# Kernel optimization log

Measured on AMD Instinct MI355X. Metric: run time of the kernel, lower is better.

The kernel has to match this reference:

```python
import jax, jax.numpy as jnp
import numpy as np

NH, NKV, D = 16, 8, 128
HID = 2048
EPS = 1e-6
ROPE_BASE = 10000.0
T = 2048


def setup_inputs() -> dict:
    key = jax.random.key(0)
    k1, k2, k3 = jax.random.split(key, 3)
    return {
        "positions": jnp.arange(T, dtype=jnp.int32),
        "hidden_states": jax.random.normal(k1, (T, HID), dtype=jnp.float32),
        "w_qkv": jax.random.normal(k2, (HID, (NH + 2 * NKV) * D), dtype=jnp.float32) * 0.02,
        "w_o": jax.random.normal(k3, (NH * D, HID), dtype=jnp.float32) * 0.02,
        "q_norm_w": jnp.ones((D,), dtype=jnp.float32),
        "k_norm_w": jnp.ones((D,), dtype=jnp.float32),
    }


def _rmsnorm(x, w):
    # per-head RMSNorm over last dim (head_dim)
    return x * jax.lax.rsqrt(jnp.mean(x * x, axis=-1, keepdims=True) + EPS) * w


def reference(positions, hidden_states, w_qkv, w_o, q_norm_w, k_norm_w):
    t = hidden_states.shape[0]
    scale = D ** -0.5

    # fused QKV projection, then split
    qkv = hidden_states @ w_qkv                       # [T, (NH+2*NKV)*D]
    q, k, v = jnp.split(qkv, [NH * D, (NH + NKV) * D], axis=-1)
    q = q.reshape(t, NH, D)
    k = k.reshape(t, NKV, D)
    v = v.reshape(t, NKV, D)

    # per-head QK RMSNorm (Qwen3)
    q = _rmsnorm(q, q_norm_w)
    k = _rmsnorm(k, k_norm_w)

    # RoPE (neox style: rotate half-split pairs)
    inv_freq = 1.0 / (ROPE_BASE ** (jnp.arange(0, D, 2, dtype=jnp.float32) / D))
    freqs = positions.astype(jnp.float32)[:, None] * inv_freq  # [T, D/2]
    cos = jnp.cos(freqs)[:, None, :]                   # [T, 1, D/2]
    sin = jnp.sin(freqs)[:, None, :]

    def rope(x):
        x1, x2 = jnp.split(x, 2, axis=-1)
        return jnp.concatenate([x1 * cos - x2 * sin, x2 * cos + x1 * sin], axis=-1)

    q = rope(q)
    k = rope(k)

    # GQA: repeat kv heads
    g = NH // NKV
    kr = jnp.repeat(k, g, axis=1)                      # [T, NH, D]
    vr = jnp.repeat(v, g, axis=1)

    # causal attention
    scores = jnp.einsum('thd,shd->hts', q, kr) * scale  # [NH, T, T]
    causal = jnp.tril(jnp.ones((t, t), dtype=bool))
    scores = jnp.where(causal[None], scores, -jnp.inf)
    probs = jax.nn.softmax(scores, axis=-1)
    o = jnp.einsum('hts,shd->thd', probs, vr).reshape(t, NH * D)

    return o @ w_o
```

## Files before the change

### kernel.cpp

```cpp
#include <hip/hip_runtime.h>
#include <math.h>

#define T_TOK 2048
#define HIDDEN 2048
#define NH 16
#define NKV 8
#define DH 128

typedef unsigned short u16;
typedef __attribute__((ext_vector_type(8))) short bf16x8;
typedef __attribute__((ext_vector_type(4))) float f32x4;

__device__ __forceinline__ u16 f2bf(float f) {
  union { float f; unsigned u; } x; x.f = f;
  unsigned r = (x.u + 0x7fffu + ((x.u >> 16) & 1u)) >> 16;
  return (u16)r;
}

__device__ __forceinline__ float bf2f(u16 v) {
  union { unsigned u; float f; } x; x.u = ((unsigned)v) << 16;
  return x.f;
}

__device__ __forceinline__ void gload16(const void* g, void* l) {
  __builtin_amdgcn_global_load_lds((const __attribute__((address_space(1))) void*)g,
                                   (__attribute__((address_space(3))) void*)l,
                                   16, 0, 0);
}

__global__ __launch_bounds__(256) void prepass(const float* __restrict__ hidden,
                                               const float* __restrict__ w_qkv,
                                               const float* __restrict__ w_o,
                                               u16* __restrict__ Xb,
                                               u16* __restrict__ WqkvT,
                                               u16* __restrict__ WoT) {
  __shared__ float tile[64][65];
  const int b = blockIdx.x;
  if (b < 4096) {
    int i = b * 256 + threadIdx.x;
    float4 v = ((const float4*)hidden)[i];
    ushort4 o;
    o.x = f2bf(v.x); o.y = f2bf(v.y); o.z = f2bf(v.z); o.w = f2bf(v.w);
    ((ushort4*)Xb)[i] = o;
    return;
  }
  const float* in; u16* out; int R, Cdim, c0, r0;
  if (b < 6144) {
    int bb = b - 4096;
    in = w_qkv; out = WqkvT; R = 2048; Cdim = 4096;
    c0 = (bb & 63) * 64; r0 = (bb >> 6) * 64;
  } else {
    int bb = b - 6144;
    in = w_o; out = WoT; R = 2048; Cdim = 2048;
    c0 = (bb & 31) * 64; r0 = (bb >> 5) * 64;
  }
  const int tx = threadIdx.x & 63, ty = threadIdx.x >> 6;
#pragma unroll
  for (int i = 0; i < 64; i += 4)
    tile[ty + i][tx] = in[(size_t)(r0 + ty + i) * Cdim + c0 + tx];
  __syncthreads();
#pragma unroll
  for (int i = 0; i < 64; i += 4)
    out[(size_t)(c0 + ty + i) * R + r0 + tx] = f2bf(tile[tx][ty + i]);
}

__global__ __launch_bounds__(256) void add_parts4(const u16* __restrict__ a,
                                                  const u16* __restrict__ b,
                                                  const u16* __restrict__ c,
                                                  const u16* __restrict__ d,
                                                  float* __restrict__ o, int n4) {
  int i = blockIdx.x * blockDim.x + threadIdx.x;
  if (i < n4) {
    ushort4 x = ((const ushort4*)a)[i], y = ((const ushort4*)b)[i];
    ushort4 u = ((const ushort4*)c)[i], v = ((const ushort4*)d)[i];
    float4 z;
    z.x = bf2f(x.x) + bf2f(y.x) + bf2f(u.x) + bf2f(v.x);
    z.y = bf2f(x.y) + bf2f(y.y) + bf2f(u.y) + bf2f(v.y);
    z.z = bf2f(x.z) + bf2f(y.z) + bf2f(u.z) + bf2f(v.z);
    z.w = bf2f(x.w) + bf2f(y.w) + bf2f(u.w) + bf2f(v.w);
    ((float4*)o)[i] = z;
  }
}

__global__ __launch_bounds__(256) void rope_vt(const u16* __restrict__ qkv0,
                                               const u16* __restrict__ qkv1,
                                               const int* __restrict__ pos,
                                               const float* __restrict__ qw,
                                               const float* __restrict__ kw,
                                               u16* __restrict__ Qg,
                                               u16* __restrict__ Kg,
                                               u16* __restrict__ Vt,
                                               unsigned* __restrict__ counter) {
  __shared__ float tile[64][65];
  const int b = blockIdx.x;
  if (b < 12288) {
    const int wave = threadIdx.x >> 6, j = threadIdx.x & 63;
    const int idx = b * 4 + wave;
    const int t = idx & 2047, slot = idx >> 11;
    const float QSC = 0.088388347648318447f * 1.4426950408889634f;
    const size_t base_i = (size_t)t * 4096 + slot * 128;
    float x1 = bf2f(qkv0[base_i + j]) + bf2f(qkv1[base_i + j]);
    float x2 = bf2f(qkv0[base_i + j + 64]) + bf2f(qkv1[base_i + j + 64]);
    float ss = x1 * x1 + x2 * x2;
#pragma unroll
    for (int m = 1; m < 64; m <<= 1) ss += __shfl_xor(ss, m);
    float r = rsqrtf(ss * (1.0f / 128.0f) + 1e-6f);
    const bool isq = slot < NH;
    const float* w = isq ? qw : kw;
    float xn1 = x1 * r * w[j], xn2 = x2 * r * w[j + 64];
    float fp = (float)pos[t];
    float inv_freq = exp2f(-(float)j * (13.287712379549449f / 64.0f));
    float ang = fp * inv_freq;
    float sn, cs;
    sincosf(ang, &sn, &cs);
    float o1 = xn1 * cs - xn2 * sn;
    float o2 = xn2 * cs + xn1 * sn;
    if (isq) {
      size_t base = ((size_t)slot * T_TOK + t) * DH;
      Qg[base + j] = f2bf(o1 * QSC); Qg[base + 64 + j] = f2bf(o2 * QSC);
    } else {
      size_t base = ((size_t)(slot - NH) * T_TOK + t) * DH;
      Kg[base + j] = f2bf(o1); Kg[base + 64 + j] = f2bf(o2);
    }
    return;
  }
  if (b == 12288 && threadIdx.x == 0) *counter = 0u;
  const int bb = b - 12288;
  const int h = bb & 7, rest = bb >> 3;
  const int t0 = (rest & 31) * 64, d0 = (rest >> 5) * 64;
  const int tx = threadIdx.x & 63, ty = threadIdx.x >> 6;
#pragma unroll
  for (int i = 0; i < 64; i += 4) {
    size_t gi = (size_t)(t0 + ty + i) * 4096 + (NH + NKV) * DH + h * DH + d0 + tx;
    tile[ty + i][tx] = bf2f(qkv0[gi]) + bf2f(qkv1[gi]);
  }
  __syncthreads();
#pragma unroll
  for (int i = 0; i < 64; i += 4)
    Vt[((size_t)h * DH + d0 + ty + i) * T_TOK + t0 + tx] = f2bf(tile[tx][ty + i]);
}

__global__ __launch_bounds__(512, 2) void gemm256(const u16* __restrict__ A,
                                                  const u16* __restrict__ Bt,
                                                  void* __restrict__ Cout,
                                                  int M, int N, int K, int lda, int ldb,
                                                  int obf16) {
  __shared__ __attribute__((aligned(128))) char lds[131072];

  const int nx = N >> 8, ny = M >> 8;
  const int flat = blockIdx.x;
  const int per = gridDim.x >> 3;
  const int swz = (flat & 7) * per + (flat >> 3);
  const int by = swz % ny;
  const int rest = swz / ny;
  const int bx = rest % nx;
  const int bz = rest / nx;
  const int m0 = by << 8, n0 = bx << 8;
  A += (size_t)bz * K;
  Bt += (size_t)bz * K;

  const int tid = threadIdx.x;
  const int wave = tid >> 6, lane = tid & 63;
  const int l15 = lane & 15, quad = lane >> 4;
  const int wr = wave >> 2, wc = wave & 3;

  size_t aoff[2], boff[2];
#pragma unroll
  for (int c = 0; c < 2; ++c) {
    int chunk = c * 512 + tid;
    int line = chunk >> 3;
    int ls8 = (chunk & 7) ^ (line & 7);
    int row = line * 2 + (ls8 >> 2);
    int ks = ls8 & 3;
    aoff[c] = (size_t)(m0 + row) * lda + ks * 8;
    boff[c] = (size_t)(n0 + row) * ldb + ks * 8;
  }

#define STAGE(tt) do {                                                  \
    char* db = lds + ((tt) & 3) * 16384 + wave * 1024;                  \
    const int kk = (tt) * 32;                                           \
    gload16(A + aoff[0] + kk, db);                                      \
    gload16(A + aoff[1] + kk, db + 8192);                               \
    gload16(Bt + boff[0] + kk, db + 65536);                             \
    gload16(Bt + boff[1] + kk, db + 65536 + 8192);                      \
  } while (0)

  const int fragoff = (l15 >> 1) * 128 +
                      (((((l15 & 1) << 2) | quad) ^ ((l15 >> 1) & 7)) << 4);

  const f32x4 zero = {0.f, 0.f, 0.f, 0.f};
  f32x4 acc[8][4];
#pragma unroll
  for (int i = 0; i < 8; ++i)
#pragma unroll
    for (int j = 0; j < 4; ++j) acc[i][j] = zero;

  const int NT = K >> 5;
  STAGE(0); STAGE(1); STAGE(2);
  asm volatile("s_waitcnt vmcnt(8)" ::: "memory");
  __builtin_amdgcn_s_barrier();

  for (int t = 0; t < NT; ++t) {
    const char* As = lds + (t & 3) * 16384 + wr * 8192 + fragoff;
    const char* Bs = lds + 65536 + (t & 3) * 16384 + wc * 4096 + fragoff;
    bf16x8 af[8], bfr[4];
#pragma unroll
    for (int mt = 0; mt < 8; ++mt) af[mt] = *(const bf16x8*)(As + mt * 1024);
#pragma unroll
    for (int nt = 0; nt < 4; ++nt) bfr[nt] = *(const bf16x8*)(Bs + nt * 1024);

    if (t + 3 < NT) STAGE(t + 3);

    __builtin_amdgcn_s_setprio(1);
#pragma unroll
    for (int mt = 0; mt < 8; ++mt)
#pragma unroll
      for (int nt = 0; nt < 4; ++nt)
        acc[mt][nt] = __builtin_amdgcn_mfma_f32_16x16x32_bf16(af[mt], bfr[nt], acc[mt][nt], 0, 0, 0);
    __builtin_amdgcn_s_setprio(0);

    const int rem = NT - 1 - t;
    if (rem >= 3)      asm volatile("s_waitcnt vmcnt(8)" ::: "memory");
    else if (rem == 2) asm volatile("s_waitcnt vmcnt(4)" ::: "memory");
    else if (rem == 1) asm volatile("s_waitcnt vmcnt(0)" ::: "memory");
    if (rem > 0) __builtin_amdgcn_s_barrier();
  }
#undef STAGE

  if (obf16) {
    u16* C = (u16*)Cout + (size_t)bz * M * N;
#pragma unroll
    for (int mt = 0; mt < 8; ++mt)
#pragma unroll
      for (int nt = 0; nt < 4; ++nt)
#pragma unroll
        for (int r = 0; r < 4; ++r)
          C[(size_t)(m0 + wr * 128 + mt * 16 + quad * 4 + r) * N + n0 + wc * 64 + nt * 16 + l15] =
              f2bf(acc[mt][nt][r]);
  } else {
    float* C = (float*)Cout + (size_t)bz * M * N;
#pragma unroll
    for (int mt = 0; mt < 8; ++mt)
#pragma unroll
      for (int nt = 0; nt < 4; ++nt)
#pragma unroll
        for (int r = 0; r < 4; ++r)
          C[(size_t)(m0 + wr * 128 + mt * 16 + quad * 4 + r) * N + n0 + wc * 64 + nt * 16 + l15] =
              acc[mt][nt][r];
  }
}

__global__ __launch_bounds__(256) void attn_kernel(const u16* __restrict__ Qg,
                                                   const u16* __restrict__ Kg,
                                                   const u16* __restrict__ Vtg,
                                                   float* __restrict__ Opart,
                                                   float* __restrict__ Lpart,
                                                   unsigned* __restrict__ counter) {
  __shared__ u16 Klds[64 * 128];
  __shared__ u16 Vlds[128 * 64];
  __shared__ u16 Plds[4][16 * 72];
  __shared__ unsigned item_s;
  const int wave = threadIdx.x >> 6, lane = threadIdx.x & 63;
  const int l15 = lane & 15, quad = lane >> 4;
  u16* Pw = &Plds[wave][0];
  const f32x4 zero = {0.f, 0.f, 0.f, 0.f};
  const float4 zero4 = {0.f, 0.f, 0.f, 0.f};

  for (;;) {
    __syncthreads();
    if (threadIdx.x == 0) item_s = atomicAdd(counter, 1u);
    __syncthreads();
    const unsigned item = item_s;
    if (item >= 1024u) break;
    const int qt = 31 - (int)(item >> 5);
    const int s  = (int)(item >> 4) & 1;
    const int h  = (int)item & 15;
    const int kvh = h >> 1;
    const int slot = (h * 32 + qt) * 2 + s;
    const int j0 = s ? (qt + 2) >> 1 : 0;
    const int j1 = s ? qt + 1 : (qt + 2) >> 1;

    float* Oslot = Opart + (size_t)slot * (64 * 128);

    if (j0 >= j1) {
      for (int t = threadIdx.x; t < 64 * 128 / 4; t += 256) ((float4*)Oslot)[t] = zero4;
      if (threadIdx.x < 64) Lpart[slot * 64 + threadIdx.x] = 0.f;
      continue;
    }

    const u16* Qh = Qg + (size_t)h * T_TOK * DH;
    const u16* Kh = Kg + (size_t)kvh * T_TOK * DH;
    const u16* Vh = Vtg + (size_t)kvh * DH * T_TOK;
    const int qrow0 = qt * 64 + wave * 16;

    bf16x8 qf[4];
#pragma unroll
    for (int ks = 0; ks < 4; ++ks)
      qf[ks] = *(const bf16x8*)(Qh + (size_t)(qrow0 + l15) * DH + ks * 32 + quad * 8);

    f32x4 oacc[8];
#pragma unroll
    for (int i = 0; i < 8; ++i) oacc[i] = zero;
    float l_i[4] = {0.f, 0.f, 0.f, 0.f};

    for (int j = j0; j < j1; ++j) {
      __syncthreads();
#pragma unroll
      for (int c = 0; c < 4; ++c) {
        int chunk = wave * 4 + c;
        int sl = chunk * 64 + lane;
        {
          int ss = sl >> 4;
          int g = (sl & 15) ^ (ss & 15);
          gload16(Kh + ((size_t)(j * 64 + ss)) * DH + g * 8, &Klds[chunk * 512]);
        }
        {
          int d = sl >> 3;
          int g = (sl & 7) ^ (d & 7);
          gload16(Vh + (size_t)d * T_TOK + j * 64 + g * 8, &Vlds[chunk * 512]);
        }
      }
      __syncthreads();

      f32x4 sacc[4];
#pragma unroll
      for (int nt = 0; nt < 4; ++nt) sacc[nt] = zero;
#pragma unroll
      for (int nt = 0; nt < 4; ++nt) {
        int sr = nt * 16 + l15;
#pragma unroll
        for (int ks = 0; ks < 4; ++ks) {
          bf16x8 kf = *(const bf16x8*)&Klds[sr * 128 + (((ks * 4 + quad) ^ (sr & 15)) * 8)];
          sacc[nt] = __builtin_amdgcn_mfma_f32_16x16x32_bf16(qf[ks], kf, sacc[nt], 0, 0, 0);
        }
      }

      if (j == qt) {
#pragma unroll
        for (int nt = 0; nt < 4; ++nt)
#pragma unroll
          for (int r = 0; r < 4; ++r) {
            int col = j * 64 + nt * 16 + l15;
            int row = qrow0 + quad * 4 + r;
            if (col > row) sacc[nt][r] = -INFINITY;
          }
      }

#pragma unroll
      for (int nt = 0; nt < 4; ++nt)
#pragma unroll
        for (int r = 0; r < 4; ++r) {
          float pv = exp2f(sacc[nt][r]);
          unsigned u = __float_as_uint(pv);
          Pw[(quad * 4 + r) * 72 + nt * 16 + l15] = (u16)(u >> 16);
          l_i[r] += __uint_as_float(u & 0xffff0000u);
        }

      bf16x8 pf[2];
#pragma unroll
      for (int ks = 0; ks < 2; ++ks)
        pf[ks] = *(const bf16x8*)&Pw[l15 * 72 + ks * 32 + quad * 8];
#pragma unroll
      for (int ot = 0; ot < 8; ++ot) {
        int d = ot * 16 + l15;
#pragma unroll
        for (int ks = 0; ks < 2; ++ks) {
          bf16x8 vf = *(const bf16x8*)&Vlds[d * 64 + (((ks * 4 + quad) ^ (d & 7)) * 8)];
          oacc[ot] = __builtin_amdgcn_mfma_f32_16x16x32_bf16(pf[ks], vf, oacc[ot], 0, 0, 0);
        }
      }
    }

#pragma unroll
    for (int ot = 0; ot < 8; ++ot)
#pragma unroll
      for (int r = 0; r < 4; ++r)
        Oslot[(wave * 16 + quad * 4 + r) * 128 + ot * 16 + l15] = oacc[ot][r];
#pragma unroll
    for (int msk = 1; msk < 16; msk <<= 1)
#pragma unroll
      for (int r = 0; r < 4; ++r) l_i[r] += __shfl_xor(l_i[r], msk);
    if (l15 == 0) {
#pragma unroll
      for (int r = 0; r < 4; ++r)
        Lpart[slot * 64 + wave * 16 + quad * 4 + r] = l_i[r];
    }
  }
}

__global__ __launch_bounds__(256) void attn_merge(const float* __restrict__ Opart,
                                                  const float* __restrict__ Lpart,
                                                  u16* __restrict__ Og) {
  const int b = blockIdx.x;
  const int h = b & 15, qt = b >> 4;
  const int slot0 = (h * 32 + qt) * 2, slot1 = slot0 + 1;
  const float4* O0 = (const float4*)(Opart + (size_t)slot0 * (64 * 128));
  const float4* O1 = (const float4*)(Opart + (size_t)slot1 * (64 * 128));
#pragma unroll
  for (int it = 0; it < 8; ++it) {
    int idx = it * 256 + threadIdx.x;
    int r = idx >> 5, c4 = idx & 31;
    float rl = 1.0f / (Lpart[slot0 * 64 + r] + Lpart[slot1 * 64 + r]);
    float4 a = O0[idx], c = O1[idx];
    int row = qt * 64 + r, col = c4 * 4;
    u16* dst = Og + (size_t)row * (NH * DH) + h * DH + col;
    dst[0] = f2bf((a.x + c.x) * rl);
    dst[1] = f2bf((a.y + c.y) * rl);
    dst[2] = f2bf((a.z + c.z) * rl);
    dst[3] = f2bf((a.w + c.w) * rl);
  }
}

extern "C" void kernel_launch(void* const* d_in, const int* in_sizes, int n_in,
                              void* d_out, int out_size, void* d_ws, size_t ws_size,
                              hipStream_t stream) {
  (void)in_sizes; (void)n_in; (void)out_size; (void)ws_size;
  const int* positions = (const int*)d_in[0];
  const float* hidden  = (const float*)d_in[1];
  const float* w_qkv   = (const float*)d_in[2];
  const float* w_o     = (const float*)d_in[3];
  const float* q_norm  = (const float*)d_in[4];
  const float* k_norm  = (const float*)d_in[5];
  float* out = (float*)d_out;

  char* ws = (char*)d_ws;
  u16*   Xb    = (u16*)(ws);
  u16*   WqkvT = (u16*)(ws + ( 8ull << 20));
  u16*   WoT   = (u16*)(ws + (24ull << 20));
  u16*   P0    = (u16*)(ws + (32ull << 20));
  u16*   P1    = P0 + (size_t)T_TOK * 4096;
  u16*   Qg    = (u16*)(ws + (64ull << 20));
  u16*   Kg    = (u16*)(ws + (72ull << 20));
  u16*   Vt    = (u16*)(ws + (76ull << 20));
  u16*   AttnO = (u16*)(ws + (80ull << 20));
  float* Opart = (float*)(ws + (32ull << 20));
  float* Lpart = (float*)(ws);
  unsigned* ctr = (unsigned*)(ws + (512ull << 10));
  u16*   G2P   = (u16*)(ws + (32ull << 20));

  prepass<<<dim3(7168), 256, 0, stream>>>(hidden, w_qkv, w_o, Xb, WqkvT, WoT);

  gemm256<<<dim3(256), 512, 0, stream>>>(
      Xb, WqkvT, P0, T_TOK, 4096, 1024, HIDDEN, HIDDEN, 1);

  rope_vt<<<dim3(12288 + 512), 256, 0, stream>>>(P0, P1, positions,
                                                 q_norm, k_norm, Qg, Kg, Vt, ctr);

  attn_kernel<<<dim3(768), 256, 0, stream>>>(Qg, Kg, Vt, Opart, Lpart, ctr);
  attn_merge<<<dim3(512), 256, 0, stream>>>(Opart, Lpart, AttnO);

  gemm256<<<dim3(256), 512, 0, stream>>>(
      AttnO, WoT, G2P, T_TOK, HIDDEN, 512, NH * DH, NH * DH, 1);
  const int n4 = T_TOK * HIDDEN / 4;
  add_parts4<<<dim3(n4 / 256), 256, 0, stream>>>(
      G2P, G2P + (size_t)T_TOK * HIDDEN, G2P + 2 * (size_t)T_TOK * HIDDEN,
      G2P + 3 * (size_t)T_TOK * HIDDEN, out, n4);
}
```

Before: 251.8 us.

## Double-buffer K/V tiles in attention kernel and prefetch the next tile

Doubles the K and V shared-memory tiles so the global-to-LDS load of tile j+1 is issued before computing on tile j. This replaces the two barriers per iteration with one wait-and-barrier at the end. Wave priority is raised around the MFMA loops, and the persistent grid shrinks from 768 to 512 blocks because the doubled LDS footprint lowers how many blocks fit per CU. The aim is to hide global load latency behind matrix math, at the cost of more LDS and fewer resident blocks.

```diff
diff --git a/kernel.cpp b/kernel.cpp
--- a/kernel.cpp
+++ b/kernel.cpp
@@ -256,8 +256,8 @@
                                                    float* __restrict__ Opart,
                                                    float* __restrict__ Lpart,
                                                    unsigned* __restrict__ counter) {
-  __shared__ u16 Klds[64 * 128];
-  __shared__ u16 Vlds[128 * 64];
+  __shared__ u16 Klds[2][64 * 128];
+  __shared__ u16 Vlds[2][128 * 64];
   __shared__ u16 Plds[4][16 * 72];
   __shared__ unsigned item_s;
   const int wave = threadIdx.x >> 6, lane = threadIdx.x & 63;
@@ -265,6 +265,20 @@
   u16* Pw = &Plds[wave][0];
   const f32x4 zero = {0.f, 0.f, 0.f, 0.f};
   const float4 zero4 = {0.f, 0.f, 0.f, 0.f};
+
+#define STAGEKV(jj, sl) do {                                            \
+    u16* Kd = &Klds[sl][0]; u16* Vd = &Vlds[sl][0];                     \
+    _Pragma("unroll")                                                   \
+    for (int c = 0; c < 4; ++c) {                                       \
+      int chunk = wave * 4 + c;                                         \
+      int sL = chunk * 64 + lane;                                       \
+      { int ss = sL >> 4;                                               \
+        int g = (sL & 15) ^ (ss & 15);                                  \
+        gload16(Kh + ((size_t)((jj) * 64 + ss)) * DH + g * 8, Kd + chunk * 512); } \
+      { int d = sL >> 3;                                                \
+        int g = (sL & 7) ^ (d & 7);                                     \
+        gload16(Vh + (size_t)d * T_TOK + (jj) * 64 + g * 8, Vd + chunk * 512); } \
+    } } while (0)
 
   for (;;) {
     __syncthreads();
@@ -303,37 +317,30 @@
     for (int i = 0; i < 8; ++i) oacc[i] = zero;
     float l_i[4] = {0.f, 0.f, 0.f, 0.f};
 
+    STAGEKV(j0, 0);
+    asm volatile("s_waitcnt vmcnt(0)" ::: "memory");
+    __builtin_amdgcn_s_barrier();
+
     for (int j = j0; j < j1; ++j) {
-      __syncthreads();
-#pragma unroll
-      for (int c = 0; c < 4; ++c) {
-        int chunk = wave * 4 + c;
-        int sl = chunk * 64 + lane;
-        {
-          int ss = sl >> 4;
-          int g = (sl & 15) ^ (ss & 15);
-          gload16(Kh + ((size_t)(j * 64 + ss)) * DH + g * 8, &Klds[chunk * 512]);
-        }
-        {
-          int d = sl >> 3;
-          int g = (sl & 7) ^ (d & 7);
-          gload16(Vh + (size_t)d * T_TOK + j * 64 + g * 8, &Vlds[chunk * 512]);
-        }
-      }
-      __syncthreads();
+      const int sl = (j - j0) & 1;
+      if (j + 1 < j1) STAGEKV(j + 1, sl ^ 1);
+      const u16* Kl = &Klds[sl][0];
+      const u16* Vl = &Vlds[sl][0];
 
       f32x4 sacc[4];
 #pragma unroll
       for (int nt = 0; nt < 4; ++nt) sacc[nt] = zero;
+      __builtin_amdgcn_s_setprio(1);
 #pragma unroll
       for (int nt = 0; nt < 4; ++nt) {
         int sr = nt * 16 + l15;
 #pragma unroll
         for (int ks = 0; ks < 4; ++ks) {
-          bf16x8 kf = *(const bf16x8*)&Klds[sr * 128 + (((ks * 4 + quad) ^ (sr & 15)) * 8)];
+          bf16x8 kf = *(const bf16x8*)&Kl[sr * 128 + (((ks * 4 + quad) ^ (sr & 15)) * 8)];
           sacc[nt] = __builtin_amdgcn_mfma_f32_16x16x32_bf16(qf[ks], kf, sacc[nt], 0, 0, 0);
         }
       }
+      __builtin_amdgcn_s_setprio(0);
 
       if (j == qt) {
 #pragma unroll
@@ -360,15 +367,22 @@
 #pragma unroll
       for (int ks = 0; ks < 2; ++ks)
         pf[ks] = *(const bf16x8*)&Pw[l15 * 72 + ks * 32 + quad * 8];
+      __builtin_amdgcn_s_setprio(1);
 #pragma unroll
       for (int ot = 0; ot < 8; ++ot) {
         int d = ot * 16 + l15;
 #pragma unroll
         for (int ks = 0; ks < 2; ++ks) {
-          bf16x8 vf = *(const bf16x8*)&Vlds[d * 64 + (((ks * 4 + quad) ^ (d & 7)) * 8)];
+          bf16x8 vf = *(const bf16x8*)&Vl[d * 64 + (((ks * 4 + quad) ^ (d & 7)) * 8)];
           oacc[ot] = __builtin_amdgcn_mfma_f32_16x16x32_bf16(pf[ks], vf, oacc[ot], 0, 0, 0);
         }
       }
+      __builtin_amdgcn_s_setprio(0);
+
+      if (j + 1 < j1) {
+        asm volatile("s_waitcnt vmcnt(0)" ::: "memory");
+        __builtin_amdgcn_s_barrier();
+      }
     }
 
 #pragma unroll
@@ -386,6 +400,7 @@
         Lpart[slot * 64 + wave * 16 + quad * 4 + r] = l_i[r];
     }
   }
+#undef STAGEKV
 }
 
 __global__ __launch_bounds__(256) void attn_merge(const float* __restrict__ Opart,
@@ -446,7 +461,7 @@
   rope_vt<<<dim3(12288 + 512), 256, 0, stream>>>(P0, P1, positions,
                                                  q_norm, k_norm, Qg, Kg, Vt, ctr);
 
-  attn_kernel<<<dim3(768), 256, 0, stream>>>(Qg, Kg, Vt, Opart, Lpart, ctr);
+  attn_kernel<<<dim3(512), 256, 0, stream>>>(Qg, Kg, Vt, Opart, Lpart, ctr);
   attn_merge<<<dim3(512), 256, 0, stream>>>(Opart, Lpart, AttnO);
 
   gemm256<<<dim3(256), 512, 0, stream>>>(
```

Result: no change. 247.4 us (-1.8%).

## Process both GQA query heads per K/V tile and rebalance attention work split

Applied to the files above, without the earlier changes.

Each attention work item now handles the two query heads that share one KV head, so every K/V tile loaded into LDS feeds twice as many MFMAs. Work is split into 4 key-range pieces for late query tiles and 2 for early ones, and the merge kernel now sums a variable number of partials. The change also adds s_setprio around the MFMA loops, sets launch_bounds to 2 blocks per CU, shrinks the grid, and moves the Q/K/V buffers in the workspace. Register pressure roughly doubles for the accumulators, which may hurt occupancy, and the Opart and Lpart layouts change for the merge step.

```diff
diff --git a/kernel.cpp b/kernel.cpp
--- a/kernel.cpp
+++ b/kernel.cpp
@@ -250,19 +250,20 @@
   }
 }
 
-__global__ __launch_bounds__(256) void attn_kernel(const u16* __restrict__ Qg,
-                                                   const u16* __restrict__ Kg,
-                                                   const u16* __restrict__ Vtg,
-                                                   float* __restrict__ Opart,
-                                                   float* __restrict__ Lpart,
-                                                   unsigned* __restrict__ counter) {
+__global__ __launch_bounds__(256, 2) void attn_kernel(const u16* __restrict__ Qg,
+                                                      const u16* __restrict__ Kg,
+                                                      const u16* __restrict__ Vtg,
+                                                      float* __restrict__ Opart,
+                                                      float* __restrict__ Lpart,
+                                                      unsigned* __restrict__ counter) {
   __shared__ u16 Klds[64 * 128];
   __shared__ u16 Vlds[128 * 64];
-  __shared__ u16 Plds[4][16 * 72];
+  __shared__ u16 Plds[4][2][16 * 72];
   __shared__ unsigned item_s;
   const int wave = threadIdx.x >> 6, lane = threadIdx.x & 63;
   const int l15 = lane & 15, quad = lane >> 4;
-  u16* Pw = &Plds[wave][0];
+  u16* Pw0 = &Plds[wave][0][0];
+  u16* Pw1 = &Plds[wave][1][0];
   const f32x4 zero = {0.f, 0.f, 0.f, 0.f};
   const float4 zero4 = {0.f, 0.f, 0.f, 0.f};
 
@@ -271,37 +272,49 @@
     if (threadIdx.x == 0) item_s = atomicAdd(counter, 1u);
     __syncthreads();
     const unsigned item = item_s;
-    if (item >= 1024u) break;
-    const int qt = 31 - (int)(item >> 5);
-    const int s  = (int)(item >> 4) & 1;
-    const int h  = (int)item & 15;
-    const int kvh = h >> 1;
-    const int slot = (h * 32 + qt) * 2 + s;
-    const int j0 = s ? (qt + 2) >> 1 : 0;
-    const int j1 = s ? qt + 1 : (qt + 2) >> 1;
-
-    float* Oslot = Opart + (size_t)slot * (64 * 128);
+    if (item >= 768u) break;
+    const int qxs = (int)(item >> 3);
+    const int kvh = (int)item & 7;
+    int qt, s, shf;
+    if (qxs < 64) { qt = 31 - (qxs >> 2); s = qxs & 3; shf = 2; }
+    else { int q2 = qxs - 64; qt = 15 - (q2 >> 1); s = q2 & 1; shf = 1; }
+    const int n = qt + 1;
+    const int j0 = (n * s) >> shf;
+    const int j1 = (n * (s + 1)) >> shf;
+    const int slot0 = (int)item * 2;
+
+    float* O0 = Opart + (size_t)slot0 * (64 * 128);
+    float* O1 = O0 + 64 * 128;
 
     if (j0 >= j1) {
-      for (int t = threadIdx.x; t < 64 * 128 / 4; t += 256) ((float4*)Oslot)[t] = zero4;
-      if (threadIdx.x < 64) Lpart[slot * 64 + threadIdx.x] = 0.f;
+      for (int t = threadIdx.x; t < 64 * 128 / 4; t += 256) {
+        ((float4*)O0)[t] = zero4; ((float4*)O1)[t] = zero4;
+      }
+      if (threadIdx.x < 64) {
+        Lpart[slot0 * 64 + threadIdx.x] = 0.f;
+        Lpart[(slot0 + 1) * 64 + threadIdx.x] = 0.f;
+      }
       continue;
     }
 
-    const u16* Qh = Qg + (size_t)h * T_TOK * DH;
+    const u16* Qh0 = Qg + (size_t)(kvh * 2) * T_TOK * DH;
+    const u16* Qh1 = Qh0 + (size_t)T_TOK * DH;
     const u16* Kh = Kg + (size_t)kvh * T_TOK * DH;
     const u16* Vh = Vtg + (size_t)kvh * DH * T_TOK;
     const int qrow0 = qt * 64 + wave * 16;
 
-    bf16x8 qf[4];
-#pragma unroll
-    for (int ks = 0; ks < 4; ++ks)
-      qf[ks] = *(const bf16x8*)(Qh + (size_t)(qrow0 + l15) * DH + ks * 32 + quad * 8);
-
-    f32x4 oacc[8];
-#pragma unroll
-    for (int i = 0; i < 8; ++i) oacc[i] = zero;
-    float l_i[4] = {0.f, 0.f, 0.f, 0.f};
+    bf16x8 qf0[4], qf1[4];
+#pragma unroll
+    for (int ks = 0; ks < 4; ++ks) {
+      qf0[ks] = *(const bf16x8*)(Qh0 + (size_t)(qrow0 + l15) * DH + ks * 32 + quad * 8);
+      qf1[ks] = *(const bf16x8*)(Qh1 + (size_t)(qrow0 + l15) * DH + ks * 32 + quad * 8);
+    }
+
+    f32x4 oacc0[8], oacc1[8];
+#pragma unroll
+    for (int i = 0; i < 8; ++i) { oacc0[i] = zero; oacc1[i] = zero; }
+    float l0[4] = {0.f, 0.f, 0.f, 0.f};
+    float l1[4] = {0.f, 0.f, 0.f, 0.f};
 
     for (int j = j0; j < j1; ++j) {
       __syncthreads();
@@ -322,18 +335,21 @@
       }
       __syncthreads();
 
-      f32x4 sacc[4];
-#pragma unroll
-      for (int nt = 0; nt < 4; ++nt) sacc[nt] = zero;
+      f32x4 s0[4], s1[4];
+#pragma unroll
+      for (int nt = 0; nt < 4; ++nt) { s0[nt] = zero; s1[nt] = zero; }
+      __builtin_amdgcn_s_setprio(1);
 #pragma unroll
       for (int nt = 0; nt < 4; ++nt) {
         int sr = nt * 16 + l15;
 #pragma unroll
         for (int ks = 0; ks < 4; ++ks) {
           bf16x8 kf = *(const bf16x8*)&Klds[sr * 128 + (((ks * 4 + quad) ^ (sr & 15)) * 8)];
-          sacc[nt] = __builtin_amdgcn_mfma_f32_16x16x32_bf16(qf[ks], kf, sacc[nt], 0, 0, 0);
+          s0[nt] = __builtin_amdgcn_mfma_f32_16x16x32_bf16(qf0[ks], kf, s0[nt], 0, 0, 0);
+          s1[nt] = __builtin_amdgcn_mfma_f32_16x16x32_bf16(qf1[ks], kf, s1[nt], 0, 0, 0);
         }
       }
+      __builtin_amdgcn_s_setprio(0);
 
       if (j == qt) {
 #pragma unroll
@@ -342,7 +358,7 @@
           for (int r = 0; r < 4; ++r) {
             int col = j * 64 + nt * 16 + l15;
             int row = qrow0 + quad * 4 + r;
-            if (col > row) sacc[nt][r] = -INFINITY;
+            if (col > row) { s0[nt][r] = -INFINITY; s1[nt][r] = -INFINITY; }
           }
       }
 
@@ -350,40 +366,56 @@
       for (int nt = 0; nt < 4; ++nt)
 #pragma unroll
         for (int r = 0; r < 4; ++r) {
-          float pv = exp2f(sacc[nt][r]);
-          unsigned u = __float_as_uint(pv);
-          Pw[(quad * 4 + r) * 72 + nt * 16 + l15] = (u16)(u >> 16);
-          l_i[r] += __uint_as_float(u & 0xffff0000u);
+          float pv0 = exp2f(s0[nt][r]);
+          unsigned u0 = __float_as_uint(pv0);
+          Pw0[(quad * 4 + r) * 72 + nt * 16 + l15] = (u16)(u0 >> 16);
+          l0[r] += __uint_as_float(u0 & 0xffff0000u);
+          float pv1 = exp2f(s1[nt][r]);
+          unsigned u1 = __float_as_uint(pv1);
+          Pw1[(quad * 4 + r) * 72 + nt * 16 + l15] = (u16)(u1 >> 16);
+          l1[r] += __uint_as_float(u1 & 0xffff0000u);
         }
 
-      bf16x8 pf[2];
-#pragma unroll
-      for (int ks = 0; ks < 2; ++ks)
-        pf[ks] = *(const bf16x8*)&Pw[l15 * 72 + ks * 32 + quad * 8];
+      bf16x8 pf0[2], pf1[2];
+#pragma unroll
+      for (int ks = 0; ks < 2; ++ks) {
+        pf0[ks] = *(const bf16x8*)&Pw0[l15 * 72 + ks * 32 + quad * 8];
+        pf1[ks] = *(const bf16x8*)&Pw1[l15 * 72 + ks * 32 + quad * 8];
+      }
+      __builtin_amdgcn_s_setprio(1);
 #pragma unroll
       for (int ot = 0; ot < 8; ++ot) {
         int d = ot * 16 + l15;
 #pragma unroll
         for (int ks = 0; ks < 2; ++ks) {
           bf16x8 vf = *(const bf16x8*)&Vlds[d * 64 + (((ks * 4 + quad) ^ (d & 7)) * 8)];
-          oacc[ot] = __builtin_amdgcn_mfma_f32_16x16x32_bf16(pf[ks], vf, oacc[ot], 0, 0, 0);
+          oacc0[ot] = __builtin_amdgcn_mfma_f32_16x16x32_bf16(pf0[ks], vf, oacc0[ot], 0, 0, 0);
+          oacc1[ot] = __builtin_amdgcn_mfma_f32_16x16x32_bf16(pf1[ks], vf, oacc1[ot], 0, 0, 0);
         }
       }
+      __builtin_amdgcn_s_setprio(0);
     }
 
 #pragma unroll
     for (int ot = 0; ot < 8; ++ot)
 #pragma unroll
-      for (int r = 0; r < 4; ++r)
-        Oslot[(wave * 16 + quad * 4 + r) * 128 + ot * 16 + l15] = oacc[ot][r];
+      for (int r = 0; r < 4; ++r) {
+        O0[(wave * 16 + quad * 4 + r) * 128 + ot * 16 + l15] = oacc0[ot][r];
+        O1[(wave * 16 + quad * 4 + r) * 128 + ot * 16 + l15] = oacc1[ot][r];
+      }
 #pragma unroll
     for (int msk = 1; msk < 16; msk <<= 1)
 #pragma unroll
-      for (int r = 0; r < 4; ++r) l_i[r] += __shfl_xor(l_i[r], msk);
+      for (int r = 0; r < 4; ++r) {
+        l0[r] += __shfl_xor(l0[r], msk);
+        l1[r] += __shfl_xor(l1[r], msk);
+      }
     if (l15 == 0) {
 #pragma unroll
-      for (int r = 0; r < 4; ++r)
-        Lpart[slot * 64 + wave * 16 + quad * 4 + r] = l_i[r];
+      for (int r = 0; r < 4; ++r) {
+        Lpart[slot0 * 64 + wave * 16 + quad * 4 + r] = l0[r];
+        Lpart[(slot0 + 1) * 64 + wave * 16 + quad * 4 + r] = l1[r];
+      }
     }
   }
 }
@@ -393,21 +425,36 @@
                                                   u16* __restrict__ Og) {
   const int b = blockIdx.x;
   const int h = b & 15, qt = b >> 4;
-  const int slot0 = (h * 32 + qt) * 2, slot1 = slot0 + 1;
-  const float4* O0 = (const float4*)(Opart + (size_t)slot0 * (64 * 128));
-  const float4* O1 = (const float4*)(Opart + (size_t)slot1 * (64 * 128));
+  const int kvh = h >> 1, hp = h & 1;
+  int ns, base_qxs;
+  if (qt >= 16) { ns = 4; base_qxs = (31 - qt) * 4; }
+  else          { ns = 2; base_qxs = 64 + (15 - qt) * 2; }
+  int sl[4];
+#pragma unroll
+  for (int s = 0; s < 4; ++s)
+    sl[s] = ((base_qxs + (s < ns ? s : 0)) * 8 + kvh) * 2 + hp;
 #pragma unroll
   for (int it = 0; it < 8; ++it) {
     int idx = it * 256 + threadIdx.x;
     int r = idx >> 5, c4 = idx & 31;
-    float rl = 1.0f / (Lpart[slot0 * 64 + r] + Lpart[slot1 * 64 + r]);
-    float4 a = O0[idx], c = O1[idx];
+    float L = Lpart[sl[0] * 64 + r] + Lpart[sl[1] * 64 + r];
+    float4 a = ((const float4*)(Opart + (size_t)sl[0] * 8192))[idx];
+    float4 c = ((const float4*)(Opart + (size_t)sl[1] * 8192))[idx];
+    float4 acc;
+    acc.x = a.x + c.x; acc.y = a.y + c.y; acc.z = a.z + c.z; acc.w = a.w + c.w;
+    if (ns == 4) {
+      L += Lpart[sl[2] * 64 + r] + Lpart[sl[3] * 64 + r];
+      float4 e = ((const float4*)(Opart + (size_t)sl[2] * 8192))[idx];
+      float4 f = ((const float4*)(Opart + (size_t)sl[3] * 8192))[idx];
+      acc.x += e.x + f.x; acc.y += e.y + f.y; acc.z += e.z + f.z; acc.w += e.w + f.w;
+    }
+    float rl = 1.0f / L;
     int row = qt * 64 + r, col = c4 * 4;
     u16* dst = Og + (size_t)row * (NH * DH) + h * DH + col;
-    dst[0] = f2bf((a.x + c.x) * rl);
-    dst[1] = f2bf((a.y + c.y) * rl);
-    dst[2] = f2bf((a.z + c.z) * rl);
-    dst[3] = f2bf((a.w + c.w) * rl);
+    dst[0] = f2bf(acc.x * rl);
+    dst[1] = f2bf(acc.y * rl);
+    dst[2] = f2bf(acc.z * rl);
+    dst[3] = f2bf(acc.w * rl);
   }
 }
 
@@ -429,9 +476,9 @@
   u16*   WoT   = (u16*)(ws + (24ull << 20));
   u16*   P0    = (u16*)(ws + (32ull << 20));
   u16*   P1    = P0 + (size_t)T_TOK * 4096;
-  u16*   Qg    = (u16*)(ws + (64ull << 20));
-  u16*   Kg    = (u16*)(ws + (72ull << 20));
-  u16*   Vt    = (u16*)(ws + (76ull << 20));
+  u16*   Qg    = (u16*)(ws + ( 8ull << 20));
+  u16*   Kg    = (u16*)(ws + (16ull << 20));
+  u16*   Vt    = (u16*)(ws + (20ull << 20));
   u16*   AttnO = (u16*)(ws + (80ull << 20));
   float* Opart = (float*)(ws + (32ull << 20));
   float* Lpart = (float*)(ws);
@@ -446,7 +493,7 @@
   rope_vt<<<dim3(12288 + 512), 256, 0, stream>>>(P0, P1, positions,
                                                  q_norm, k_norm, Qg, Kg, Vt, ctr);
 
-  attn_kernel<<<dim3(768), 256, 0, stream>>>(Qg, Kg, Vt, Opart, Lpart, ctr);
+  attn_kernel<<<dim3(512), 256, 0, stream>>>(Qg, Kg, Vt, Opart, Lpart, ctr);
   attn_merge<<<dim3(512), 256, 0, stream>>>(Opart, Lpart, AttnO);
 
   gemm256<<<dim3(256), 512, 0, stream>>>(
```

After: 267.2 us. +6.1%, slower.
